# Performance work log

Hardware: AMD Instinct MI355X
Metric: run time of the kernel (lower is better)

The kernel has to match this reference:

```python
import jax, jax.numpy as jnp
import numpy as np

B, L, D = 4096, 200, 64
N_ITEMS, N_USERS, N_RATINGS = 100000, 100000, 5


def setup_inputs() -> dict:
    key = jax.random.key(0)
    ks = jax.random.split(key, 10)
    nodes = jax.random.randint(ks[0], (B,), 0, N_USERS)
    history_uv = jax.random.randint(ks[1], (B, L), 0, N_ITEMS)
    history_r = jax.random.randint(ks[2], (B, L), 0, N_RATINGS)
    s = 1.0 / np.sqrt(D)
    v2e = jax.random.normal(ks[3], (N_ITEMS, D), dtype=jnp.float32)
    r2e = jax.random.normal(ks[4], (N_RATINGS, D), dtype=jnp.float32)
    # torch Linear: weight is [out, in]
    w1_W = jax.random.uniform(ks[5], (D, 2 * D), dtype=jnp.float32, minval=-s, maxval=s)
    w1_b = jax.random.uniform(ks[6], (D,), dtype=jnp.float32, minval=-s, maxval=s)
    w2_W = jax.random.uniform(ks[7], (D, D), dtype=jnp.float32, minval=-s, maxval=s)
    w2_b = jax.random.uniform(ks[8], (D,), dtype=jnp.float32, minval=-s, maxval=s)
    return {
        "v2e": v2e, "r2e": r2e,
        "w1_W": w1_W, "w1_b": w1_b, "w2_W": w2_W, "w2_b": w2_b,
        "nodes": nodes, "history_uv": history_uv, "history_r": history_r,
    }


def reference(v2e, r2e, w1_W, w1_b, w2_W, w2_b, nodes, history_uv, history_r):
    # Gather item and rating embeddings for every (node, history slot): [B, L, D]
    e_uv = v2e[history_uv]
    e_r = r2e[history_r]
    # concat -> [B, L, 2D], two-layer MLP with ReLU
    x = jnp.concatenate([e_uv, e_r], axis=-1)
    h = jax.nn.relu(jnp.einsum("bli,oi->blo", x, w1_W) + w1_b)
    o = jax.nn.relu(jnp.einsum("bli,oi->blo", h, w2_W) + w2_b)
    # uv=True branch: plain mean over the history dimension (nodes/u2e unused)
    return jnp.mean(o, axis=1)  # [B, D]
```

## Files before the change

### kernel.cpp

```cpp
#include <hip/hip_runtime.h>

#define NITEMS 100000
#define NRATE  5
#define BB     4096
#define LL     200
#define DD     64

typedef short short8 __attribute__((ext_vector_type(8)));
typedef short short4v __attribute__((ext_vector_type(4)));
typedef float f32x4  __attribute__((ext_vector_type(4)));

static __device__ __forceinline__ short f2bf(float f) {
  unsigned u = __builtin_bit_cast(unsigned, f);
  u += 0x7fffu + ((u >> 16) & 1u);
  return (short)(u >> 16);
}
static __device__ __forceinline__ float bf2f(short s) {
  return __builtin_bit_cast(float, (unsigned)((unsigned short)s) << 16);
}

__global__ __launch_bounds__(256) void k_prep(
    const float* __restrict__ r2e, const float* __restrict__ w1W,
    const float* __restrict__ w1b, const float* __restrict__ w2W,
    short* __restrict__ w1abf, short* __restrict__ w2bf,
    float* __restrict__ pre_r5)
{
  const int tid = threadIdx.x;
  const int blk = blockIdx.x;
  if (blk < 4) {
    const int g = blk * 256 + tid;
    const int base = g * 4;
    const int o = base >> 6, k = base & 63;
    const float4 v = *reinterpret_cast<const float4*>(w1W + o * 128 + k);
    short4v s = {f2bf(v.x), f2bf(v.y), f2bf(v.z), f2bf(v.w)};
    *reinterpret_cast<short4v*>(w1abf + base) = s;
  } else if (blk < 8) {
    const int g = (blk - 4) * 256 + tid;
    const int base = g * 4;
    const float4 v = *reinterpret_cast<const float4*>(w2W + base);
    short4v s = {f2bf(v.x), f2bf(v.y), f2bf(v.z), f2bf(v.w)};
    *reinterpret_cast<short4v*>(w2bf + base) = s;
  } else {
    const int r = blk - 8;
    if (tid < 64) {
      const int o = tid;
      const float4* wr = reinterpret_cast<const float4*>(w1W + o * 128 + 64);
      const float4* rr = reinterpret_cast<const float4*>(r2e + r * 64);
      float s = w1b[o];
#pragma unroll
      for (int q = 0; q < 16; ++q) {
        const float4 a = wr[q], b = rr[q];
        s += a.x * b.x + a.y * b.y + a.z * b.z + a.w * b.w;
      }
      pre_r5[r * 64 + o] = s;
    }
  }
}

__global__ __launch_bounds__(256) void k_pre_uv(
    const float* __restrict__ v2e, const short* __restrict__ w1abf,
    short* __restrict__ pre_uv)
{
  __shared__ __align__(16) short sD[4][16][72];
  const int tid  = threadIdx.x;
  const int wave = tid >> 6, lane = tid & 63;
  const int n = lane & 15, quad = lane >> 4;
  const int ibase = blockIdx.x * 64 + wave * 16;

  short8 bfr[2][4];
#pragma unroll
  for (int nt = 0; nt < 4; ++nt)
#pragma unroll
    for (int kh = 0; kh < 2; ++kh)
      bfr[kh][nt] = *reinterpret_cast<const short8*>(
          w1abf + (nt * 16 + n) * 64 + kh * 32 + quad * 8);

  const int arow = min(ibase + n, NITEMS - 1);
  short8 afr[2];
#pragma unroll
  for (int kh = 0; kh < 2; ++kh) {
    const float4* p = reinterpret_cast<const float4*>(
        v2e + (size_t)arow * 64 + kh * 32 + quad * 8);
    const float4 x0 = p[0], x1 = p[1];
    short8 a;
    a[0] = f2bf(x0.x); a[1] = f2bf(x0.y); a[2] = f2bf(x0.z); a[3] = f2bf(x0.w);
    a[4] = f2bf(x1.x); a[5] = f2bf(x1.y); a[6] = f2bf(x1.z); a[7] = f2bf(x1.w);
    afr[kh] = a;
  }

  f32x4 d[4];
#pragma unroll
  for (int nt = 0; nt < 4; ++nt) {
    f32x4 z = {0.f, 0.f, 0.f, 0.f};
    z = __builtin_amdgcn_mfma_f32_16x16x32_bf16(afr[0], bfr[0][nt], z, 0, 0, 0);
    z = __builtin_amdgcn_mfma_f32_16x16x32_bf16(afr[1], bfr[1][nt], z, 0, 0, 0);
    d[nt] = z;
  }

#pragma unroll
  for (int nt = 0; nt < 4; ++nt)
#pragma unroll
    for (int r = 0; r < 4; ++r)
      sD[wave][quad * 4 + r][nt * 16 + n] = f2bf(d[nt][r]);

  __syncthreads();

  const int srow = lane >> 2, chunk = lane & 3;
  const short8 v0 = *reinterpret_cast<const short8*>(&sD[wave][srow][chunk * 16]);
  const short8 v1 = *reinterpret_cast<const short8*>(&sD[wave][srow][chunk * 16 + 8]);
  const int item = ibase + srow;
  if (item < NITEMS) {
    short* dst = pre_uv + (size_t)item * 64 + chunk * 16;
    *reinterpret_cast<short8*>(dst) = v0;
    *reinterpret_cast<short8*>(dst + 8) = v1;
  }
}

__global__ __launch_bounds__(256) void k_main(
    const short* __restrict__ pre_uv, const float* __restrict__ pre_r5,
    const short* __restrict__ w2bf, const float* __restrict__ w2b,
    const int* __restrict__ huv, const int* __restrict__ hrr,
    float* __restrict__ out)
{
  __shared__ __align__(16) float s_r5[5 * 68];
  __shared__ float red[4][64];

  const int tid  = threadIdx.x;
  const int wave = tid >> 6, lane = tid & 63;
  const int n = lane & 15, quad = lane >> 4;
  const int b = blockIdx.x;

  for (int idx = tid; idx < 5 * 64; idx += 256)
    s_r5[(idx >> 6) * 68 + (idx & 63)] = pre_r5[idx];

  const int* hu = huv + b * LL;
  const int* hr = hrr + b * LL;
  int iv[4], ir[4];
#pragma unroll
  for (int t = 0; t < 4; ++t) {
    const int lc = min(wave * 16 + t * 64 + n, LL - 1);
    iv[t] = hu[lc];
    ir[t] = hr[lc];
  }

  short8 bfr[2][4];
#pragma unroll
  for (int nt = 0; nt < 4; ++nt)
#pragma unroll
    for (int kh = 0; kh < 2; ++kh)
      bfr[kh][nt] = *reinterpret_cast<const short8*>(
          w2bf + (nt * 16 + n) * 64 + kh * 32 + quad * 8);

  float bias[4];
#pragma unroll
  for (int nt = 0; nt < 4; ++nt) bias[nt] = w2b[nt * 16 + n];

  short8 u[4][2];
#pragma unroll
  for (int t = 0; t < 4; ++t)
#pragma unroll
    for (int kh = 0; kh < 2; ++kh)
      u[t][kh] = *reinterpret_cast<const short8*>(
          pre_uv + (size_t)iv[t] * 64 + kh * 32 + quad * 8);

  __syncthreads();

  float acc[4] = {0.f, 0.f, 0.f, 0.f};
#pragma unroll
  for (int t = 0; t < 4; ++t) {
    short8 afr[2];
#pragma unroll
    for (int kh = 0; kh < 2; ++kh) {
      const float4* rp = reinterpret_cast<const float4*>(
          s_r5 + ir[t] * 68 + kh * 32 + quad * 8);
      const float4 r0 = rp[0], r1 = rp[1];
      const float rv[8] = {r0.x, r0.y, r0.z, r0.w, r1.x, r1.y, r1.z, r1.w};
      short8 a;
#pragma unroll
      for (int j = 0; j < 8; ++j) {
        const float h = bf2f(u[t][kh][j]) + rv[j];
        a[j] = f2bf(fmaxf(h, 0.f));
      }
      afr[kh] = a;
    }

    f32x4 d[4];
#pragma unroll
    for (int nt = 0; nt < 4; ++nt) {
      f32x4 z = {0.f, 0.f, 0.f, 0.f};
      z = __builtin_amdgcn_mfma_f32_16x16x32_bf16(afr[0], bfr[0][nt], z, 0, 0, 0);
      z = __builtin_amdgcn_mfma_f32_16x16x32_bf16(afr[1], bfr[1][nt], z, 0, 0, 0);
      d[nt] = z;
    }

    const int lbase = wave * 16 + t * 64;
#pragma unroll
    for (int nt = 0; nt < 4; ++nt)
#pragma unroll
      for (int r = 0; r < 4; ++r) {
        const int rl = lbase + quad * 4 + r;
        const float v = fmaxf(d[nt][r] + bias[nt], 0.f);
        acc[nt] += (rl < LL) ? v : 0.f;
      }
  }

#pragma unroll
  for (int nt = 0; nt < 4; ++nt) {
    float v = acc[nt];
    v += __shfl_xor(v, 16, 64);
    v += __shfl_xor(v, 32, 64);
    acc[nt] = v;
  }

  if (lane < 16) {
#pragma unroll
    for (int nt = 0; nt < 4; ++nt) red[wave][nt * 16 + lane] = acc[nt];
  }
  __syncthreads();
  if (tid < 64) {
    const float s = red[0][tid] + red[1][tid] + red[2][tid] + red[3][tid];
    out[b * 64 + tid] = s * (1.0f / (float)LL);
  }
}

__global__ __launch_bounds__(256) void k_fallback(
    const float* __restrict__ v2e, const float* __restrict__ r2e,
    const float* __restrict__ w1W, const float* __restrict__ w1b,
    const float* __restrict__ w2W, const float* __restrict__ w2b,
    const int* __restrict__ huv, const int* __restrict__ hrr,
    float* __restrict__ out)
{
  __shared__ float sw1[64][129];
  __shared__ float sw2[64][65];
  __shared__ float sx[4][128];
  __shared__ float sh[4][64];
  __shared__ float red[4][64];

  const int tid = threadIdx.x;
  const int wave = tid >> 6, lane = tid & 63;
  const int b = blockIdx.x;

  for (int idx = tid; idx < 64 * 128; idx += 256) sw1[idx >> 7][idx & 127] = w1W[idx];
  for (int idx = tid; idx < 64 * 64; idx += 256) sw2[idx >> 6][idx & 63] = w2W[idx];
  __syncthreads();

  const float b1o = w1b[lane], b2o = w2b[lane];
  float acc = 0.f;

  for (int l = wave; l < LL; l += 4) {
    const int iv = huv[b * LL + l];
    const int ir = hrr[b * LL + l];
    sx[wave][lane]      = v2e[iv * 64 + lane];
    sx[wave][64 + lane] = r2e[ir * 64 + lane];
    __syncthreads();
    float h = b1o;
    for (int i = 0; i < 128; ++i) h += sx[wave][i] * sw1[lane][i];
    sh[wave][lane] = fmaxf(h, 0.f);
    __syncthreads();
    float o = b2o;
    for (int i = 0; i < 64; ++i) o += sh[wave][i] * sw2[lane][i];
    acc += fmaxf(o, 0.f);
  }

  red[wave][lane] = acc;
  __syncthreads();
  if (tid < 64) {
    const float s = red[0][tid] + red[1][tid] + red[2][tid] + red[3][tid];
    out[b * 64 + tid] = s * (1.0f / (float)LL);
  }
}

extern "C" void kernel_launch(void* const* d_in, const int* in_sizes, int n_in,
                              void* d_out, int out_size, void* d_ws, size_t ws_size,
                              hipStream_t stream) {
  (void)in_sizes; (void)n_in; (void)out_size;
  const float* v2e = (const float*)d_in[0];
  const float* r2e = (const float*)d_in[1];
  const float* w1W = (const float*)d_in[2];
  const float* w1b = (const float*)d_in[3];
  const float* w2W = (const float*)d_in[4];
  const float* w2b = (const float*)d_in[5];
  const int* huv = (const int*)d_in[7];
  const int* hrr = (const int*)d_in[8];
  float* out = (float*)d_out;

  const size_t OFF_R5  = (size_t)NITEMS * 64 * sizeof(short);
  const size_t OFF_W2  = OFF_R5 + NRATE * 64 * sizeof(float);
  const size_t OFF_W1A = OFF_W2 + 64 * 64 * sizeof(short);
  const size_t NEED    = OFF_W1A + 64 * 64 * sizeof(short);

  if (ws_size >= NEED) {
    short* pre_uv = (short*)d_ws;
    float* pre_r5 = (float*)((char*)d_ws + OFF_R5);
    short* w2bf   = (short*)((char*)d_ws + OFF_W2);
    short* w1abf  = (short*)((char*)d_ws + OFF_W1A);

    k_prep<<<13, 256, 0, stream>>>(r2e, w1W, w1b, w2W, w1abf, w2bf, pre_r5);
    k_pre_uv<<<(NITEMS + 63) / 64, 256, 0, stream>>>(v2e, w1abf, pre_uv);
    k_main<<<BB, 256, 0, stream>>>(pre_uv, pre_r5, w2bf, w2b, huv, hrr, out);
  } else {
    k_fallback<<<BB, 256, 0, stream>>>(v2e, r2e, w1W, w1b, w2W, w2b, huv, hrr, out);
  }
}
```

Baseline: 128.5 us.

## Fuse prep kernels, permute hidden layout, and skip padded history tiles

Merges the weight-prep and item-precompute kernels into one launch. Each block now converts W1 on the fly, processes 256 items per block with register prefetch of the next tile, and writes MFMA results directly in a k-permuted layout without staging through shared memory. The W2 columns and the rating bias table are permuted to match that layout. The main kernel also skips the fully padded fourth history tile on three of its four waves. This removes a launch and the LDS round trip, and cuts redundant gathers, at the cost of 4-element scattered stores and an unbalanced fourth wave.

```diff
diff --git a/kernel.cpp b/kernel.cpp
--- a/kernel.cpp
+++ b/kernel.cpp
@@ -5,10 +5,11 @@
 #define BB     4096
 #define LL     200
 #define DD     64
-
-typedef short short8 __attribute__((ext_vector_type(8)));
+#define NBUV   391
+
+typedef short short8  __attribute__((ext_vector_type(8)));
 typedef short short4v __attribute__((ext_vector_type(4)));
-typedef float f32x4  __attribute__((ext_vector_type(4)));
+typedef float f32x4   __attribute__((ext_vector_type(4)));
 
 static __device__ __forceinline__ short f2bf(float f) {
   unsigned u = __builtin_bit_cast(unsigned, f);
@@ -18,32 +19,28 @@
 static __device__ __forceinline__ float bf2f(short s) {
   return __builtin_bit_cast(float, (unsigned)((unsigned short)s) << 16);
 }
-
-__global__ __launch_bounds__(256) void k_prep(
-    const float* __restrict__ r2e, const float* __restrict__ w1W,
-    const float* __restrict__ w1b, const float* __restrict__ w2W,
-    short* __restrict__ w1abf, short* __restrict__ w2bf,
-    float* __restrict__ pre_r5)
+static __device__ __forceinline__ int kperm(int p) {
+  return ((p & 3) << 4) | (p >> 2);
+}
+
+__global__ __launch_bounds__(256) void k_pre(
+    const float* __restrict__ v2e, const float* __restrict__ r2e,
+    const float* __restrict__ w1W, const float* __restrict__ w1b,
+    const float* __restrict__ w2W,
+    short* __restrict__ pre_uv, short* __restrict__ w2p,
+    float* __restrict__ r5p)
 {
   const int tid = threadIdx.x;
   const int blk = blockIdx.x;
-  if (blk < 4) {
-    const int g = blk * 256 + tid;
-    const int base = g * 4;
-    const int o = base >> 6, k = base & 63;
-    const float4 v = *reinterpret_cast<const float4*>(w1W + o * 128 + k);
-    short4v s = {f2bf(v.x), f2bf(v.y), f2bf(v.z), f2bf(v.w)};
-    *reinterpret_cast<short4v*>(w1abf + base) = s;
-  } else if (blk < 8) {
-    const int g = (blk - 4) * 256 + tid;
-    const int base = g * 4;
-    const float4 v = *reinterpret_cast<const float4*>(w2W + base);
-    short4v s = {f2bf(v.x), f2bf(v.y), f2bf(v.z), f2bf(v.w)};
-    *reinterpret_cast<short4v*>(w2bf + base) = s;
-  } else {
-    const int r = blk - 8;
-    if (tid < 64) {
-      const int o = tid;
+
+  if (blk >= NBUV) {
+    for (int idx = tid; idx < 64 * 64; idx += 256) {
+      const int o = idx >> 6, p = idx & 63;
+      w2p[idx] = f2bf(w2W[o * 64 + kperm(p)]);
+    }
+    for (int idx = tid; idx < NRATE * 64; idx += 256) {
+      const int r = idx >> 6, p = idx & 63;
+      const int o = kperm(p);
       const float4* wr = reinterpret_cast<const float4*>(w1W + o * 128 + 64);
       const float4* rr = reinterpret_cast<const float4*>(r2e + r * 64);
       float s = w1b[o];
@@ -52,73 +49,86 @@
         const float4 a = wr[q], b = rr[q];
         s += a.x * b.x + a.y * b.y + a.z * b.z + a.w * b.w;
       }
-      pre_r5[r * 64 + o] = s;
-    }
-  }
-}
-
-__global__ __launch_bounds__(256) void k_pre_uv(
-    const float* __restrict__ v2e, const short* __restrict__ w1abf,
-    short* __restrict__ pre_uv)
-{
-  __shared__ __align__(16) short sD[4][16][72];
-  const int tid  = threadIdx.x;
+      r5p[r * 64 + p] = s;
+    }
+    return;
+  }
+
   const int wave = tid >> 6, lane = tid & 63;
   const int n = lane & 15, quad = lane >> 4;
-  const int ibase = blockIdx.x * 64 + wave * 16;
 
   short8 bfr[2][4];
 #pragma unroll
   for (int nt = 0; nt < 4; ++nt)
 #pragma unroll
-    for (int kh = 0; kh < 2; ++kh)
-      bfr[kh][nt] = *reinterpret_cast<const short8*>(
-          w1abf + (nt * 16 + n) * 64 + kh * 32 + quad * 8);
-
-  const int arow = min(ibase + n, NITEMS - 1);
-  short8 afr[2];
-#pragma unroll
-  for (int kh = 0; kh < 2; ++kh) {
-    const float4* p = reinterpret_cast<const float4*>(
-        v2e + (size_t)arow * 64 + kh * 32 + quad * 8);
-    const float4 x0 = p[0], x1 = p[1];
-    short8 a;
-    a[0] = f2bf(x0.x); a[1] = f2bf(x0.y); a[2] = f2bf(x0.z); a[3] = f2bf(x0.w);
-    a[4] = f2bf(x1.x); a[5] = f2bf(x1.y); a[6] = f2bf(x1.z); a[7] = f2bf(x1.w);
-    afr[kh] = a;
-  }
-
-  f32x4 d[4];
-#pragma unroll
-  for (int nt = 0; nt < 4; ++nt) {
-    f32x4 z = {0.f, 0.f, 0.f, 0.f};
-    z = __builtin_amdgcn_mfma_f32_16x16x32_bf16(afr[0], bfr[0][nt], z, 0, 0, 0);
-    z = __builtin_amdgcn_mfma_f32_16x16x32_bf16(afr[1], bfr[1][nt], z, 0, 0, 0);
-    d[nt] = z;
-  }
-
-#pragma unroll
-  for (int nt = 0; nt < 4; ++nt)
-#pragma unroll
-    for (int r = 0; r < 4; ++r)
-      sD[wave][quad * 4 + r][nt * 16 + n] = f2bf(d[nt][r]);
-
-  __syncthreads();
-
-  const int srow = lane >> 2, chunk = lane & 3;
-  const short8 v0 = *reinterpret_cast<const short8*>(&sD[wave][srow][chunk * 16]);
-  const short8 v1 = *reinterpret_cast<const short8*>(&sD[wave][srow][chunk * 16 + 8]);
-  const int item = ibase + srow;
-  if (item < NITEMS) {
-    short* dst = pre_uv + (size_t)item * 64 + chunk * 16;
-    *reinterpret_cast<short8*>(dst) = v0;
-    *reinterpret_cast<short8*>(dst + 8) = v1;
+    for (int kh = 0; kh < 2; ++kh) {
+      const float4* p = reinterpret_cast<const float4*>(
+          w1W + (nt * 16 + n) * 128 + kh * 32 + quad * 8);
+      const float4 x0 = p[0], x1 = p[1];
+      short8 f;
+      f[0] = f2bf(x0.x); f[1] = f2bf(x0.y); f[2] = f2bf(x0.z); f[3] = f2bf(x0.w);
+      f[4] = f2bf(x1.x); f[5] = f2bf(x1.y); f[6] = f2bf(x1.z); f[7] = f2bf(x1.w);
+      bfr[kh][nt] = f;
+    }
+
+  const int ibase_w = blk * 256 + wave * 64;
+
+  float4 cur0, cur1, cur2, cur3;
+  {
+    const int row = min(ibase_w + n, NITEMS - 1);
+    const float4* p = reinterpret_cast<const float4*>(v2e + (size_t)row * 64 + quad * 8);
+    cur0 = p[0]; cur1 = p[1];
+    const float4* q = reinterpret_cast<const float4*>(v2e + (size_t)row * 64 + 32 + quad * 8);
+    cur2 = q[0]; cur3 = q[1];
+  }
+
+#pragma unroll
+  for (int it = 0; it < 4; ++it) {
+    float4 nx0, nx1, nx2, nx3;
+    if (it < 3) {
+      const int row = min(ibase_w + (it + 1) * 16 + n, NITEMS - 1);
+      const float4* p = reinterpret_cast<const float4*>(v2e + (size_t)row * 64 + quad * 8);
+      nx0 = p[0]; nx1 = p[1];
+      const float4* q = reinterpret_cast<const float4*>(v2e + (size_t)row * 64 + 32 + quad * 8);
+      nx2 = q[0]; nx3 = q[1];
+    }
+
+    short8 afr[2];
+    {
+      short8 a;
+      a[0] = f2bf(cur0.x); a[1] = f2bf(cur0.y); a[2] = f2bf(cur0.z); a[3] = f2bf(cur0.w);
+      a[4] = f2bf(cur1.x); a[5] = f2bf(cur1.y); a[6] = f2bf(cur1.z); a[7] = f2bf(cur1.w);
+      afr[0] = a;
+      a[0] = f2bf(cur2.x); a[1] = f2bf(cur2.y); a[2] = f2bf(cur2.z); a[3] = f2bf(cur2.w);
+      a[4] = f2bf(cur3.x); a[5] = f2bf(cur3.y); a[6] = f2bf(cur3.z); a[7] = f2bf(cur3.w);
+      afr[1] = a;
+    }
+
+    f32x4 d[4];
+#pragma unroll
+    for (int nt = 0; nt < 4; ++nt) {
+      f32x4 z = {0.f, 0.f, 0.f, 0.f};
+      z = __builtin_amdgcn_mfma_f32_16x16x32_bf16(afr[0], bfr[0][nt], z, 0, 0, 0);
+      z = __builtin_amdgcn_mfma_f32_16x16x32_bf16(afr[1], bfr[1][nt], z, 0, 0, 0);
+      d[nt] = z;
+    }
+
+#pragma unroll
+    for (int r = 0; r < 4; ++r) {
+      const int item = ibase_w + it * 16 + quad * 4 + r;
+      if (item < NITEMS) {
+        short4v s = {f2bf(d[0][r]), f2bf(d[1][r]), f2bf(d[2][r]), f2bf(d[3][r])};
+        *reinterpret_cast<short4v*>(pre_uv + (size_t)item * 64 + n * 4) = s;
+      }
+    }
+
+    if (it < 3) { cur0 = nx0; cur1 = nx1; cur2 = nx2; cur3 = nx3; }
   }
 }
 
 __global__ __launch_bounds__(256) void k_main(
-    const short* __restrict__ pre_uv, const float* __restrict__ pre_r5,
-    const short* __restrict__ w2bf, const float* __restrict__ w2b,
+    const short* __restrict__ pre_uv, const float* __restrict__ r5p,
+    const short* __restrict__ w2p, const float* __restrict__ w2b,
     const int* __restrict__ huv, const int* __restrict__ hrr,
     float* __restrict__ out)
 {
@@ -129,19 +139,21 @@
   const int wave = tid >> 6, lane = tid & 63;
   const int n = lane & 15, quad = lane >> 4;
   const int b = blockIdx.x;
+  const int ntiles = (wave == 0) ? 4 : 3;
 
   for (int idx = tid; idx < 5 * 64; idx += 256)
-    s_r5[(idx >> 6) * 68 + (idx & 63)] = pre_r5[idx];
+    s_r5[(idx >> 6) * 68 + (idx & 63)] = r5p[idx];
 
   const int* hu = huv + b * LL;
   const int* hr = hrr + b * LL;
-  int iv[4], ir[4];
-#pragma unroll
-  for (int t = 0; t < 4; ++t) {
-    const int lc = min(wave * 16 + t * 64 + n, LL - 1);
-    iv[t] = hu[lc];
-    ir[t] = hr[lc];
-  }
+  int iv[4] = {0, 0, 0, 0}, ir[4] = {0, 0, 0, 0};
+#pragma unroll
+  for (int t = 0; t < 4; ++t)
+    if (t < ntiles) {
+      const int lc = min(wave * 16 + t * 64 + n, LL - 1);
+      iv[t] = hu[lc];
+      ir[t] = hr[lc];
+    }
 
   short8 bfr[2][4];
 #pragma unroll
@@ -149,7 +161,7 @@
 #pragma unroll
     for (int kh = 0; kh < 2; ++kh)
       bfr[kh][nt] = *reinterpret_cast<const short8*>(
-          w2bf + (nt * 16 + n) * 64 + kh * 32 + quad * 8);
+          w2p + (nt * 16 + n) * 64 + kh * 32 + quad * 8);
 
   float bias[4];
 #pragma unroll
@@ -158,16 +170,18 @@
   short8 u[4][2];
 #pragma unroll
   for (int t = 0; t < 4; ++t)
-#pragma unroll
-    for (int kh = 0; kh < 2; ++kh)
-      u[t][kh] = *reinterpret_cast<const short8*>(
-          pre_uv + (size_t)iv[t] * 64 + kh * 32 + quad * 8);
+    if (t < ntiles)
+#pragma unroll
+      for (int kh = 0; kh < 2; ++kh)
+        u[t][kh] = *reinterpret_cast<const short8*>(
+            pre_uv + (size_t)iv[t] * 64 + kh * 32 + quad * 8);
 
   __syncthreads();
 
   float acc[4] = {0.f, 0.f, 0.f, 0.f};
 #pragma unroll
   for (int t = 0; t < 4; ++t) {
+    if (t >= ntiles) continue;
     short8 afr[2];
 #pragma unroll
     for (int kh = 0; kh < 2; ++kh) {
@@ -284,20 +298,17 @@
   const int* hrr = (const int*)d_in[8];
   float* out = (float*)d_out;
 
-  const size_t OFF_R5  = (size_t)NITEMS * 64 * sizeof(short);
-  const size_t OFF_W2  = OFF_R5 + NRATE * 64 * sizeof(float);
-  const size_t OFF_W1A = OFF_W2 + 64 * 64 * sizeof(short);
-  const size_t NEED    = OFF_W1A + 64 * 64 * sizeof(short);
+  const size_t OFF_R5 = (size_t)NITEMS * 64 * sizeof(short);
+  const size_t OFF_W2 = OFF_R5 + NRATE * 64 * sizeof(float);
+  const size_t NEED   = OFF_W2 + 64 * 64 * sizeof(short);
 
   if (ws_size >= NEED) {
     short* pre_uv = (short*)d_ws;
-    float* pre_r5 = (float*)((char*)d_ws + OFF_R5);
-    short* w2bf   = (short*)((char*)d_ws + OFF_W2);
-    short* w1abf  = (short*)((char*)d_ws + OFF_W1A);
-
-    k_prep<<<13, 256, 0, stream>>>(r2e, w1W, w1b, w2W, w1abf, w2bf, pre_r5);
-    k_pre_uv<<<(NITEMS + 63) / 64, 256, 0, stream>>>(v2e, w1abf, pre_uv);
-    k_main<<<BB, 256, 0, stream>>>(pre_uv, pre_r5, w2bf, w2b, huv, hrr, out);
+    float* r5p    = (float*)((char*)d_ws + OFF_R5);
+    short* w2p    = (short*)((char*)d_ws + OFF_W2);
+
+    k_pre<<<NBUV + 1, 256, 0, stream>>>(v2e, r2e, w1W, w1b, w2W, pre_uv, w2p, r5p);
+    k_main<<<BB, 256, 0, stream>>>(pre_uv, r5p, w2p, w2b, huv, hrr, out);
   } else {
     k_fallback<<<BB, 256, 0, stream>>>(v2e, r2e, w1W, w1b, w2W, w2b, huv, hrr, out);
   }
```

After: 125.0 us. -2.7%, faster.
